# Performance work log

Measured on AMD Instinct MI355X. Metric: run time of the kernel, lower is better.

## Reference

```python
import jax, jax.numpy as jnp
import numpy as np

N, D, N_CLASSES = 8192, 512, 128
POS_MARGIN = 1.0  # default path: sample_method=None, Dynamic_margin=None


def setup_inputs() -> dict:
    key = jax.random.key(0)
    k1, k2 = jax.random.split(key)
    x = jax.random.normal(k1, (N, D), dtype=jnp.float32)
    # metric-learning embeddings are L2-normalized so sim in [-1, 1]
    x = x / jnp.linalg.norm(x, axis=1, keepdims=True)
    targets = jax.random.randint(k2, (N,), 0, N_CLASSES, dtype=jnp.int64)
    return {"inputs": x, "targets": targets, "nonorm": 0}


def reference(inputs, targets, nonorm):
    n = inputs.shape[0]
    sim = jnp.matmul(inputs, inputs.T)                      # [n, n]
    same = targets[:, None] == targets[None, :]             # [n, n]
    pos_mask = same & (sim < POS_MARGIN)                    # drops self-sim == 1
    neg_mask = ~same

    # per-row masked log-sum-exp (sort in original is irrelevant to the sums)
    pos_sum = jnp.sum(jnp.where(pos_mask, jnp.exp(1.0 - sim), 0.0), axis=1)
    neg_sum = jnp.sum(jnp.where(neg_mask, jnp.exp(sim), 0.0), axis=1)
    pos_loss = jnp.log(pos_sum)
    neg_loss = jnp.log(neg_sum)

    has_neg = jnp.any(neg_mask, axis=1)                     # rows w/o negs are skipped
    loss = jnp.sum(jnp.where(has_neg, pos_loss + neg_loss, 0.0)) / n
    prec = jnp.mean(1.0 - has_neg.astype(jnp.float32))      # fraction of skipped rows

    # torch code reports means of the LAST row's pos/neg pairs
    last_pos = pos_mask[-1]
    last_neg = neg_mask[-1]
    mean_pos_sim = jnp.sum(jnp.where(last_pos, sim[-1], 0.0)) / jnp.sum(last_pos)
    mean_neg_sim = jnp.sum(jnp.where(last_neg, sim[-1], 0.0)) / jnp.sum(last_neg)
    return loss, prec, mean_pos_sim, mean_neg_sim
```

## Files before the change

### kernel.cpp

```cpp
#include <hip/hip_runtime.h>
#include <math.h>

#define N_ 8192
#define D_ 512
#define NC_ 128
#define T_ 64
#define BK_ 64
#define KSTEPS 8

typedef __attribute__((ext_vector_type(8))) short bf16x8;
typedef __attribute__((ext_vector_type(4))) float f32x4;
typedef __attribute__((ext_vector_type(4))) unsigned short us4;

static __device__ __forceinline__ unsigned short f2bf(float f) {
    union { float f; unsigned u; } c; c.f = f;
    unsigned u = c.u;
    u += 0x7fffu + ((u >> 16) & 1u);
    return (unsigned short)(u >> 16);
}

__global__ __launch_bounds__(256) void k_pre(const float* __restrict__ x,
                                             unsigned short* __restrict__ xb,
                                             double* __restrict__ gd,
                                             int* __restrict__ gi) {
    const int bid = blockIdx.x;
    const int tid = threadIdx.x;
    if (bid == 0 && tid == 0) {
        atomicExch((unsigned long long*)&gd[0], 0ull);
        atomicExch((unsigned long long*)&gd[1], 0ull);
        atomicExch((unsigned long long*)&gd[2], 0ull);
        atomicExch(&gi[0], 0); atomicExch(&gi[1], 0);
        atomicExch(&gi[2], 0); atomicExch(&gi[3], 0);
    }
    int i = bid * 256 + tid;
    float4 v = reinterpret_cast<const float4*>(x)[i];
    us4 o = { f2bf(v.x), f2bf(v.y), f2bf(v.z), f2bf(v.w) };
    reinterpret_cast<us4*>(xb)[i] = o;
}

__global__ __launch_bounds__(256, 2) void k_main(const unsigned short* __restrict__ xb,
                                                 const int* __restrict__ tg,
                                                 float* __restrict__ bufP,
                                                 float* __restrict__ bufN) {
    __shared__ alignas(16) unsigned short As[2][128 * 64];
    __shared__ alignas(16) unsigned short Bs[2][128 * 64];

    const int tid  = threadIdx.x;
    const int w    = tid >> 6;
    const int lane = tid & 63;
    const int q    = lane >> 4;
    const int l15  = lane & 15;
    const int wrow = w >> 1;
    const int wcol = w & 1;

    const int bswz = (blockIdx.x & 7) * 260 + (blockIdx.x >> 3);

    int rem = bswz;
    int it = 0;
    while (rem >= (T_ - it)) { rem -= (T_ - it); it++; }
    const int jt = it + rem;
    const int row0 = it * 128;
    const int col0 = jt * 128;

    auto stage_tile = [&](int p, int kt) {
        const int k0 = kt * BK_;
#pragma unroll
        for (int itr = 0; itr < 4; ++itr) {
            int gs = (itr * 4 + w) * 64 + lane;
            int r  = gs >> 3;
            int s  = gs & 7;
            int g  = s ^ (r & 7);
            const unsigned short* ga = xb + (size_t)(row0 + r) * D_ + k0 + g * 8;
            const unsigned short* gb = xb + (size_t)(col0 + r) * D_ + k0 + g * 8;
            __builtin_amdgcn_global_load_lds(
                (const __attribute__((address_space(1))) void*)ga,
                (__attribute__((address_space(3))) void*)(&As[p][0] + (itr * 4 + w) * 512),
                16, 0, 0);
            __builtin_amdgcn_global_load_lds(
                (const __attribute__((address_space(1))) void*)gb,
                (__attribute__((address_space(3))) void*)(&Bs[p][0] + (itr * 4 + w) * 512),
                16, 0, 0);
        }
    };

    f32x4 acc[4][4];
#pragma unroll
    for (int mi = 0; mi < 4; ++mi)
#pragma unroll
        for (int ni = 0; ni < 4; ++ni)
            acc[mi][ni] = (f32x4){0.f, 0.f, 0.f, 0.f};

    auto compute_tile = [&](int p) {
#pragma unroll
        for (int kc = 0; kc < 2; ++kc) {
            bf16x8 aF[4], bF[4];
#pragma unroll
            for (int mi = 0; mi < 4; ++mi) {
                int rA = wrow * 64 + mi * 16 + l15;
                int sl = (kc * 4 + q) ^ (rA & 7);
                aF[mi] = *reinterpret_cast<const bf16x8*>(&As[p][0] + rA * 64 + sl * 8);
            }
#pragma unroll
            for (int ni = 0; ni < 4; ++ni) {
                int rB = wcol * 64 + ni * 16 + l15;
                int sl = (kc * 4 + q) ^ (rB & 7);
                bF[ni] = *reinterpret_cast<const bf16x8*>(&Bs[p][0] + rB * 64 + sl * 8);
            }
            asm volatile("s_waitcnt lgkmcnt(0)" ::: "memory");
            __builtin_amdgcn_sched_barrier(0);
            __builtin_amdgcn_s_setprio(1);
#pragma unroll
            for (int mi = 0; mi < 4; ++mi)
#pragma unroll
                for (int ni = 0; ni < 4; ++ni)
                    acc[mi][ni] = __builtin_amdgcn_mfma_f32_16x16x32_bf16(
                        aF[mi], bF[ni], acc[mi][ni], 0, 0, 0);
            __builtin_amdgcn_s_setprio(0);
        }
    };

#define TILE(P, KS, DOSTAGE, VMN)                                         \
    do {                                                                  \
        asm volatile("s_waitcnt vmcnt(" #VMN ")" ::: "memory");           \
        __builtin_amdgcn_s_barrier();                                     \
        __builtin_amdgcn_sched_barrier(0);                                \
        compute_tile(P);                                                  \
        __builtin_amdgcn_s_barrier();                                     \
        __builtin_amdgcn_sched_barrier(0);                                \
        if (DOSTAGE) stage_tile(P, (KS) + 2);                             \
    } while (0)

    stage_tile(0, 0);
    stage_tile(1, 1);

    TILE(0, 0, 1, 8);
    TILE(1, 1, 1, 8);
    TILE(0, 2, 1, 8);
    TILE(1, 3, 1, 8);
    TILE(0, 4, 1, 8);
    TILE(1, 5, 1, 8);
    TILE(0, 6, 0, 8);
    TILE(1, 7, 0, 0);
#undef TILE

    int tC[4];
#pragma unroll
    for (int ni = 0; ni < 4; ++ni)
        tC[ni] = tg[col0 + wcol * 64 + ni * 16 + l15];

    float ps[4][4], ns[4][4];
    float cps[4], cns[4];
    int tR[4][4];
#pragma unroll
    for (int mi = 0; mi < 4; ++mi)
#pragma unroll
        for (int r = 0; r < 4; ++r) {
            ps[mi][r] = 0.f; ns[mi][r] = 0.f;
            tR[mi][r] = tg[row0 + wrow * 64 + mi * 16 + q * 4 + r];
        }
#pragma unroll
    for (int ni = 0; ni < 4; ++ni) { cps[ni] = 0.f; cns[ni] = 0.f; }

#pragma unroll
    for (int mi = 0; mi < 4; ++mi)
#pragma unroll
        for (int ni = 0; ni < 4; ++ni)
#pragma unroll
            for (int r = 0; r < 4; ++r) {
                float s = acc[mi][ni][r];
                bool same = (tR[mi][r] == tC[ni]);
                float e = __expf(same ? 1.0f - s : s);
                float pe = (same && (s < 1.0f)) ? e : 0.0f;
                float ne = same ? 0.0f : e;
                ps[mi][r] += pe; ns[mi][r] += ne;
                cps[ni]   += pe; cns[ni]   += ne;
            }

    float* scr = (float*)As;
#pragma unroll
    for (int mi = 0; mi < 4; ++mi)
#pragma unroll
        for (int r = 0; r < 4; ++r) {
            float p = ps[mi][r];
            float n = ns[mi][r];
#pragma unroll
            for (int m = 1; m < 16; m <<= 1) {
                p += __shfl_xor(p, m, 64);
                n += __shfl_xor(n, m, 64);
            }
            if (l15 == 0) {
                int rloc = wrow * 64 + mi * 16 + q * 4 + r;
                scr[wcol * 128 + rloc]       = p;
                scr[256 + wcol * 128 + rloc] = n;
            }
        }

#pragma unroll
    for (int ni = 0; ni < 4; ++ni) {
        float p = cps[ni];
        float n = cns[ni];
        p += __shfl_xor(p, 16, 64); p += __shfl_xor(p, 32, 64);
        n += __shfl_xor(n, 16, 64); n += __shfl_xor(n, 32, 64);
        if (q == 0) {
            int cloc = wcol * 64 + ni * 16 + l15;
            scr[512 + wrow * 128 + cloc] = p;
            scr[768 + wrow * 128 + cloc] = n;
        }
    }
    __syncthreads();

    if (tid < 128) {
        int r = tid;
        size_t off = ((size_t)it * T_ + jt) * 128 + r;
        bufP[off] = scr[r]       + scr[128 + r];
        bufN[off] = scr[256 + r] + scr[384 + r];
    } else if (jt != it) {
        int c = tid - 128;
        size_t off = ((size_t)jt * T_ + it) * 128 + c;
        bufP[off] = scr[512 + c] + scr[640 + c];
        bufN[off] = scr[768 + c] + scr[896 + c];
    }
}

__global__ __launch_bounds__(256) void k_post(const float* __restrict__ bufP,
                                              const float* __restrict__ bufN,
                                              const int* __restrict__ tg,
                                              const float* __restrict__ x,
                                              double* __restrict__ gd,
                                              int* __restrict__ gi,
                                              float* __restrict__ out) {
    __shared__ int lh[NC_];
    __shared__ float sv[256];
    __shared__ double Rd[256], Pd[256], Nd[256];
    __shared__ int Ri[256], Pc[256], Nc[256];
    const int t   = blockIdx.x;
    const int tid = threadIdx.x;

    if (tid < NC_) lh[tid] = 0;
    __syncthreads();
#pragma unroll
    for (int i = 0; i < 32; ++i) atomicAdd(&lh[tg[i * 256 + tid]], 1);
    __syncthreads();

    const int half = tid >> 7;
    const int r    = tid & 127;
    const float* buf  = half ? bufN : bufP;
    const float* base = buf + (size_t)t * T_ * 128 + r;
    float s = 0.f;
#pragma unroll
    for (int o = 0; o < T_; ++o) s += base[o * 128];
    sv[tid] = s;
    __syncthreads();

    double rd = 0.0; int ri = 0;
    if (tid < 128) {
        int row = t * 128 + tid;
        bool ok = lh[tg[row]] < N_;
        rd = ok ? (double)(logf(sv[tid]) + logf(sv[128 + tid])) : 0.0;
        ri = ok ? 0 : 1;
    }

    const int wv   = tid >> 6;
    const int lane = tid & 63;
    const int tlast = tg[N_ - 1];
    const float* xl = x + (size_t)(N_ - 1) * D_;
    double pd = 0.0, nd = 0.0;
    int pc = 0, nc = 0;
    for (int rep = 0; rep < 32; ++rep) {
        int row = t * 128 + rep * 4 + wv;
        const float* xj = x + (size_t)row * D_;
        double acc = 0.0;
#pragma unroll
        for (int itk = 0; itk < 8; ++itk) {
            int k = itk * 64 + lane;
            acc += (double)xl[k] * (double)xj[k];
        }
#pragma unroll
        for (int m = 32; m >= 1; m >>= 1) acc += __shfl_xor(acc, m, 64);
        if (lane == 0) {
            int tgr = tg[row];
            if (tgr == tlast) { if (acc < 1.0) { pd += acc; pc++; } }
            else              { nd += acc; nc++; }
        }
    }

    Rd[tid] = rd; Ri[tid] = ri;
    Pd[tid] = pd; Pc[tid] = pc;
    Nd[tid] = nd; Nc[tid] = nc;
    __syncthreads();
    for (int st = 128; st >= 1; st >>= 1) {
        if (tid < st) {
            Rd[tid] += Rd[tid + st]; Pd[tid] += Pd[tid + st]; Nd[tid] += Nd[tid + st];
            Ri[tid] += Ri[tid + st]; Pc[tid] += Pc[tid + st]; Nc[tid] += Nc[tid + st];
        }
        __syncthreads();
    }

    if (tid == 0) {
        atomicAdd(&gd[0], Rd[0]);
        atomicAdd(&gd[1], Pd[0]);
        atomicAdd(&gd[2], Nd[0]);
        atomicAdd(&gi[0], Ri[0]);
        atomicAdd(&gi[1], Pc[0]);
        atomicAdd(&gi[2], Nc[0]);
        __threadfence();
        int old = atomicAdd(&gi[3], 1);
        if ((old & 63) == 63) {
            double A = atomicAdd(&gd[0], 0.0);
            double B = atomicAdd(&gd[1], 0.0);
            double C = atomicAdd(&gd[2], 0.0);
            int U = atomicAdd(&gi[0], 0);
            int V = atomicAdd(&gi[1], 0);
            int Y = atomicAdd(&gi[2], 0);
            out[0] = (float)(A / (double)N_);
            out[1] = (float)U / (float)N_;
            out[2] = (float)(B / (double)V);
            out[3] = (float)(C / (double)Y);
        }
    }
}

extern "C" void kernel_launch(void* const* d_in, const int* in_sizes, int n_in,
                              void* d_out, int out_size, void* d_ws, size_t ws_size,
                              hipStream_t stream) {
    const float* x  = (const float*)d_in[0];
    const int*   tg = (const int*)d_in[1];
    char* ws = (char*)d_ws;

    unsigned short* xb = (unsigned short*)ws;
    const size_t XB = (size_t)N_ * D_ * 2;
    float*  bufP = (float*)(ws + XB);
    float*  bufN = (float*)(ws + XB + 2097152);
    double* gd   = (double*)(ws + XB + 4194304);
    int*    gi   = (int*)(ws + XB + 4194304 + 64);

    const int nblk_tri = T_ * (T_ + 1) / 2;

    hipLaunchKernelGGL(k_pre, dim3((N_ * D_) / (256 * 4)), dim3(256), 0, stream,
                       x, xb, gd, gi);
    hipLaunchKernelGGL(k_main, dim3(nblk_tri), dim3(256), 0, stream, xb, tg, bufP, bufN);
    hipLaunchKernelGGL(k_post, dim3(T_), dim3(256), 0, stream,
                       bufP, bufN, tg, x, gd, gi, (float*)d_out);
}
```

Baseline: 166.9 us.

## Move last-row similarity and class histogram work from k_post into k_pre

The fp64 dot products of the last row against all rows, and the per-block class histograms, now run in extra blocks of the preprocessing kernel, spread over thousands of blocks. Before, they ran serially inside only 64 k_post blocks. k_post now just sums 32 partial histograms and reads precomputed similarities. This shortens the tail kernel that had low parallelism, at the cost of extra workspace traffic and a larger k_pre grid. Beyond the new workspace layout, the only other change is a stricter final-block check.

```diff
diff --git a/kernel.cpp b/kernel.cpp
--- a/kernel.cpp
+++ b/kernel.cpp
@@ -21,6 +21,9 @@
 
 __global__ __launch_bounds__(256) void k_pre(const float* __restrict__ x,
                                              unsigned short* __restrict__ xb,
+                                             const int* __restrict__ tg,
+                                             double* __restrict__ sim_last,
+                                             int* __restrict__ hist32,
                                              double* __restrict__ gd,
                                              int* __restrict__ gi) {
     const int bid = blockIdx.x;
@@ -32,10 +35,34 @@
         atomicExch(&gi[0], 0); atomicExch(&gi[1], 0);
         atomicExch(&gi[2], 0); atomicExch(&gi[3], 0);
     }
-    int i = bid * 256 + tid;
-    float4 v = reinterpret_cast<const float4*>(x)[i];
-    us4 o = { f2bf(v.x), f2bf(v.y), f2bf(v.z), f2bf(v.w) };
-    reinterpret_cast<us4*>(xb)[i] = o;
+    if (bid < 4096) {
+        int i = bid * 256 + tid;
+        float4 v = reinterpret_cast<const float4*>(x)[i];
+        us4 o = { f2bf(v.x), f2bf(v.y), f2bf(v.z), f2bf(v.w) };
+        reinterpret_cast<us4*>(xb)[i] = o;
+    } else if (bid < 6144) {
+        int j    = (bid - 4096) * 4 + (tid >> 6);
+        int lane = tid & 63;
+        const float* xl = x + (size_t)(N_ - 1) * D_;
+        const float* xj = x + (size_t)j * D_;
+        double acc = 0.0;
+#pragma unroll
+        for (int it = 0; it < 8; ++it) {
+            int k = it * 64 + lane;
+            acc += (double)xl[k] * (double)xj[k];
+        }
+#pragma unroll
+        for (int m = 32; m >= 1; m >>= 1) acc += __shfl_xor(acc, m, 64);
+        if (lane == 0) sim_last[j] = acc;
+    } else {
+        __shared__ int lh[NC_];
+        int b = bid - 6144;
+        if (tid < NC_) lh[tid] = 0;
+        __syncthreads();
+        atomicAdd(&lh[tg[b * 256 + tid]], 1);
+        __syncthreads();
+        if (tid < NC_) hist32[b * NC_ + tid] = lh[tid];
+    }
 }
 
 __global__ __launch_bounds__(256, 2) void k_main(const unsigned short* __restrict__ xb,
@@ -225,7 +252,8 @@
 __global__ __launch_bounds__(256) void k_post(const float* __restrict__ bufP,
                                               const float* __restrict__ bufN,
                                               const int* __restrict__ tg,
-                                              const float* __restrict__ x,
+                                              const int* __restrict__ hist32,
+                                              const double* __restrict__ sim_last,
                                               double* __restrict__ gd,
                                               int* __restrict__ gi,
                                               float* __restrict__ out) {
@@ -236,11 +264,12 @@
     const int t   = blockIdx.x;
     const int tid = threadIdx.x;
 
-    if (tid < NC_) lh[tid] = 0;
-    __syncthreads();
-#pragma unroll
-    for (int i = 0; i < 32; ++i) atomicAdd(&lh[tg[i * 256 + tid]], 1);
-    __syncthreads();
+    if (tid < NC_) {
+        int a = 0;
+#pragma unroll
+        for (int b = 0; b < 32; ++b) a += hist32[b * NC_ + tid];
+        lh[tid] = a;
+    }
 
     const int half = tid >> 7;
     const int r    = tid & 127;
@@ -252,36 +281,17 @@
     sv[tid] = s;
     __syncthreads();
 
-    double rd = 0.0; int ri = 0;
+    double rd = 0.0, pd = 0.0, nd = 0.0;
+    int ri = 0, pc = 0, nc = 0;
     if (tid < 128) {
         int row = t * 128 + tid;
         bool ok = lh[tg[row]] < N_;
         rd = ok ? (double)(logf(sv[tid]) + logf(sv[128 + tid])) : 0.0;
         ri = ok ? 0 : 1;
-    }
-
-    const int wv   = tid >> 6;
-    const int lane = tid & 63;
-    const int tlast = tg[N_ - 1];
-    const float* xl = x + (size_t)(N_ - 1) * D_;
-    double pd = 0.0, nd = 0.0;
-    int pc = 0, nc = 0;
-    for (int rep = 0; rep < 32; ++rep) {
-        int row = t * 128 + rep * 4 + wv;
-        const float* xj = x + (size_t)row * D_;
-        double acc = 0.0;
-#pragma unroll
-        for (int itk = 0; itk < 8; ++itk) {
-            int k = itk * 64 + lane;
-            acc += (double)xl[k] * (double)xj[k];
-        }
-#pragma unroll
-        for (int m = 32; m >= 1; m >>= 1) acc += __shfl_xor(acc, m, 64);
-        if (lane == 0) {
-            int tgr = tg[row];
-            if (tgr == tlast) { if (acc < 1.0) { pd += acc; pc++; } }
-            else              { nd += acc; nc++; }
-        }
+        double sl = sim_last[row];
+        int tlast = tg[N_ - 1];
+        if (tg[row] == tlast) { if (sl < 1.0) { pd = sl; pc = 1; } }
+        else                  { nd = sl; nc = 1; }
     }
 
     Rd[tid] = rd; Ri[tid] = ri;
@@ -305,7 +315,7 @@
         atomicAdd(&gi[2], Nc[0]);
         __threadfence();
         int old = atomicAdd(&gi[3], 1);
-        if ((old & 63) == 63) {
+        if (old == 63) {
             double A = atomicAdd(&gd[0], 0.0);
             double B = atomicAdd(&gd[1], 0.0);
             double C = atomicAdd(&gd[2], 0.0);
@@ -331,14 +341,16 @@
     const size_t XB = (size_t)N_ * D_ * 2;
     float*  bufP = (float*)(ws + XB);
     float*  bufN = (float*)(ws + XB + 2097152);
-    double* gd   = (double*)(ws + XB + 4194304);
-    int*    gi   = (int*)(ws + XB + 4194304 + 64);
+    double* sim_last = (double*)(ws + XB + 4194304);
+    int*    hist32   = (int*)(ws + XB + 4194304 + 65536);
+    double* gd   = (double*)(ws + XB + 4194304 + 65536 + 16384);
+    int*    gi   = (int*)(ws + XB + 4194304 + 65536 + 16384 + 64);
 
     const int nblk_tri = T_ * (T_ + 1) / 2;
 
-    hipLaunchKernelGGL(k_pre, dim3((N_ * D_) / (256 * 4)), dim3(256), 0, stream,
-                       x, xb, gd, gi);
+    hipLaunchKernelGGL(k_pre, dim3(4096 + 2048 + 32), dim3(256), 0, stream,
+                       x, xb, tg, sim_last, hist32, gd, gi);
     hipLaunchKernelGGL(k_main, dim3(nblk_tri), dim3(256), 0, stream, xb, tg, bufP, bufN);
-    hipLaunchKernelGGL(k_post, dim3(T_), dim3(256), 0, stream,
-                       bufP, bufN, tg, x, gd, gi, (float*)d_out);
-}
+    hipLaunchKernelGGL(k_post, dim3(64), dim3(256), 0, stream,
+                       bufP, bufN, tg, hist32, sim_last, gd, gi, (float*)d_out);
+}
```

New measurement: 149.4 us. -10.5%, faster.
